# Optimization experiments

Measured on AMD Instinct MI355X. Metric: run time of the kernel, lower is better.

## Reference

```python
import jax, jax.numpy as jnp
import numpy as np

B, N_PER, D_IN, D_OUT, E_PER = 64, 256, 256, 128, 8192  # graphs, nodes/graph, in feat, out feat (=clusters K), edges/graph
EPS = 1e-12


def _sage(h, src, dst, W, b):
    # DenseSAGEConv (mean aggregator): h [n,Din], src/dst [E]
    agg = jnp.zeros_like(h).at[dst].add(h[src])                 # sum of in-neighbor messages
    deg = jnp.zeros((h.shape[0],), h.dtype).at[dst].add(1.0)
    agg = agg / jnp.maximum(deg, 1.0)[:, None]                  # mean aggregation
    z = jnp.concatenate([h, agg], axis=-1) @ W + b              # Linear(2*Din -> Dout)
    z = z / jnp.maximum(jnp.linalg.norm(z, axis=-1, keepdims=True), EPS)  # F.normalize(p=2)
    return jax.nn.relu(z)                                       # activation


def setup_inputs() -> dict:
    key = jax.random.key(0)
    ks = jax.random.split(key, 5)
    h = jax.random.normal(ks[0], (B, N_PER, D_IN), jnp.float32)
    edge_src = jax.random.randint(ks[1], (B, E_PER), 0, N_PER)
    edge_dst = jax.random.randint(ks[2], (B, E_PER), 0, N_PER)
    s = 1.0 / np.sqrt(2 * D_IN)
    W_feat = jax.random.uniform(ks[3], (2 * D_IN, D_OUT), jnp.float32, -s, s)
    b_feat = jnp.zeros((D_OUT,), jnp.float32)
    W_pool = jax.random.uniform(ks[4], (2 * D_IN, D_OUT), jnp.float32, -s, s)
    b_pool = jnp.zeros((D_OUT,), jnp.float32)
    return {"h": h, "edge_src": edge_src, "edge_dst": edge_dst,
            "W_feat": W_feat, "b_feat": b_feat, "W_pool": W_pool, "b_pool": b_pool}


def reference(h, edge_src, edge_dst, W_feat, b_feat, W_pool, b_pool):
    sage = jax.vmap(_sage, in_axes=(0, 0, 0, None, None))
    feat = sage(h, edge_src, edge_dst, W_feat, b_feat)                          # [B,n,K]
    assign = jax.nn.softmax(sage(h, edge_src, edge_dst, W_pool, b_pool), -1)    # [B,n,K]
    # h = assign^T @ feat, per graph (equivalent to block_diag(assign)^T @ stacked feat)
    h_pool = jnp.einsum('bnk,bnd->bkd', assign, feat).reshape(B * D_OUT, D_OUT)  # [B*K, Dout]
    # adj_new = S^T A S per graph; A[dst,src]=1 per edge -> sum_e outer(S[dst_e], S[src_e])
    s_dst = jnp.take_along_axis(assign, edge_dst[:, :, None], axis=1)           # [B,E,K]
    s_src = jnp.take_along_axis(assign, edge_src[:, :, None], axis=1)           # [B,E,K]
    blocks = jnp.einsum('bek,bel->bkl', s_dst, s_src)                           # [B,K,K]
    # cross-graph blocks are exactly zero in the batched graph -> block-diagonal dense adj
    adj_new = jax.scipy.linalg.block_diag(*blocks)                              # [B*K, B*K]
    return adj_new, h_pool
```

## Files before the change

### kernel.cpp

```cpp
#include <hip/hip_runtime.h>
#include <hip/hip_bf16.h>
#include <stdint.h>

#define BG 64
#define NP 256
#define DI 256
#define DO 128
#define EP 8192


typedef __attribute__((ext_vector_type(8))) short short8;
typedef __attribute__((ext_vector_type(4))) short short4v;
typedef __attribute__((ext_vector_type(4))) float float4v;

__device__ __forceinline__ int ldi(const void* p, size_t i, int i64) {
  return i64 ? (int)((const long long*)p)[i] : ((const int*)p)[i];
}

__device__ __forceinline__ short f2b(float x) {
  union { float f; unsigned u; } c; c.f = x;
  unsigned r = c.u + 0x7FFFu + ((c.u >> 16) & 1u);
  return (short)(r >> 16);
}
__device__ __forceinline__ float b2f(short b) {
  union { unsigned u; float f; } c; c.u = ((unsigned)(unsigned short)b) << 16;
  return c.f;
}

__device__ __forceinline__ int vote_i64(const void* esrc) {
  const uint32_t* ew = (const uint32_t*)esrc;
  int i64 = 1;
#pragma unroll
  for (int j = 0; j < 8; ++j)
    if (ew[2 * j + 1] != 0) i64 = 0;
  return i64;
}

__global__ __launch_bounds__(256) void k_scatter(const void* __restrict__ esrc,
                                                 const void* __restrict__ edst,
                                                 float* __restrict__ A,
                                                 short* __restrict__ Abf,
                                                 float* __restrict__ deg) {
  __shared__ float Asl[64][256];
  int b = blockIdx.y, rq = blockIdx.x, t = threadIdx.x;
  float4* Az = (float4*)&Asl[0][0];
  for (int i = t; i < 64 * 256 / 4; i += 256) Az[i] = make_float4(0.f, 0.f, 0.f, 0.f);
  int i64 = vote_i64(esrc);
  __syncthreads();
  const size_t base = (size_t)b * EP;
  for (int e = t; e < EP; e += 256) {
    int si = ldi(esrc, base + e, i64) & (NP - 1);
    int di = ldi(edst, base + e, i64) & (NP - 1);
    if ((di >> 6) == rq) atomicAdd(&Asl[di & 63][si], 1.0f);
  }
  __syncthreads();
  int wv = t >> 6, ln = t & 63;
#pragma unroll
  for (int k = 0; k < 16; ++k) {
    int r = k * 4 + wv;
    float4 v = *(float4*)&Asl[r][ln * 4];
    int gr = rq * 64 + r;
    size_t o = ((size_t)b * NP + gr) * NP + ln * 4;
    *(float4*)&A[o] = v;
    short tmp[4] = { f2b(v.x), f2b(v.y), f2b(v.z), f2b(v.w) };
    *(short4v*)&Abf[o] = *(short4v*)tmp;
    float s = v.x + v.y + v.z + v.w;
    s += __shfl_xor(s, 1);  s += __shfl_xor(s, 2);  s += __shfl_xor(s, 4);
    s += __shfl_xor(s, 8);  s += __shfl_xor(s, 16); s += __shfl_xor(s, 32);
    if (ln == 0) deg[b * NP + gr] = s;
  }
}

__global__ __launch_bounds__(256) void k_htr(const float* __restrict__ h,
                                             short* __restrict__ hThi,
                                             short* __restrict__ hTlo) {
  __shared__ float T[64][65];
  int b = blockIdx.z, n0 = blockIdx.x * 64, f0 = blockIdx.y * 64;
  int t = threadIdx.x;
  int r = t >> 4, c4 = (t & 15) * 4;
#pragma unroll
  for (int i = 0; i < 4; ++i) {
    float4 v = *(const float4*)&h[((size_t)b * NP + n0 + i * 16 + r) * DI + f0 + c4];
    T[i * 16 + r][c4 + 0] = v.x; T[i * 16 + r][c4 + 1] = v.y;
    T[i * 16 + r][c4 + 2] = v.z; T[i * 16 + r][c4 + 3] = v.w;
  }
  __syncthreads();
#pragma unroll
  for (int i = 0; i < 4; ++i) {
    int f = i * 16 + r;
    short hi4[4], lo4[4];
#pragma unroll
    for (int j = 0; j < 4; ++j) {
      float x = T[c4 + j][f];
      short hb = f2b(x);
      hi4[j] = hb;
      lo4[j] = f2b(x - b2f(hb));
    }
    size_t o = ((size_t)b * DI + f0 + f) * NP + n0 + c4;
    *(short4v*)&hThi[o] = *(short4v*)hi4;
    *(short4v*)&hTlo[o] = *(short4v*)lo4;
  }
}

__global__ __launch_bounds__(256) void k_gemm_agg(const short* __restrict__ Abf,
                                                  const short* __restrict__ hThi,
                                                  const short* __restrict__ hTlo,
                                                  const float* __restrict__ deg,
                                                  float* __restrict__ agg) {
  int b = blockIdx.y, r0 = blockIdx.x * 32, t = threadIdx.x;
  int wave = t >> 6, lane = t & 63, rt = wave & 1, fh = wave >> 1;
  int m = lane & 15, q = lane >> 4;
  float4v acc[8];
#pragma unroll
  for (int i = 0; i < 8; ++i) acc[i] = (float4v){0.f, 0.f, 0.f, 0.f};
  const short* Ar = &Abf[((size_t)b * NP + r0 + rt * 16 + m) * NP];
  for (int kc = 0; kc < NP; kc += 32) {
    short8 af = *(const short8*)&Ar[kc + q * 8];
#pragma unroll
    for (int tt = 0; tt < 8; ++tt) {
      int f = fh * 128 + tt * 16 + m;
      short8 bh = *(const short8*)&hThi[((size_t)b * DI + f) * NP + kc + q * 8];
      short8 bl = *(const short8*)&hTlo[((size_t)b * DI + f) * NP + kc + q * 8];
      acc[tt] = __builtin_amdgcn_mfma_f32_16x16x32_bf16(af, bh, acc[tt], 0, 0, 0);
      acc[tt] = __builtin_amdgcn_mfma_f32_16x16x32_bf16(af, bl, acc[tt], 0, 0, 0);
    }
  }
#pragma unroll
  for (int reg = 0; reg < 4; ++reg) {
    int row = r0 + rt * 16 + q * 4 + reg;
    float sc = 1.0f / fmaxf(deg[b * NP + row], 1.0f);
#pragma unroll
    for (int tt = 0; tt < 8; ++tt)
      agg[((size_t)b * NP + row) * DI + fh * 128 + tt * 16 + m] = acc[tt][reg] * sc;
  }
}

__global__ __launch_bounds__(256) void k_wt(const float* __restrict__ Wf,
                                            const float* __restrict__ Wp,
                                            short* __restrict__ Wt) {
  __shared__ __align__(16) float T[32][132];
  int b = blockIdx.x;
  int head = b >> 4;
  int k0 = (b & 15) * 32;
  const float* W = head ? Wp : Wf;
  int t = threadIdx.x;
  {
    int k = t >> 3, fs = (t & 7) * 16;
    const float* src = &W[(size_t)(k0 + k) * DO + fs];
#pragma unroll
    for (int j = 0; j < 4; ++j)
      *(float4*)&T[k][fs + j * 4] = *(const float4*)(src + j * 4);
  }
  __syncthreads();
  int f = t & 127, kh = (t >> 7) * 16;
  __align__(16) short tmp[16];
#pragma unroll
  for (int i = 0; i < 16; ++i) tmp[i] = f2b(T[kh + i][f]);
  short* dst = &Wt[((size_t)head * DO + f) * 512 + k0 + kh];
  *(short8*)dst = *(short8*)&tmp[0];
  *(short8*)(dst + 8) = *(short8*)&tmp[8];
}

__global__ __launch_bounds__(256) void k_zepi_mfma(const float* __restrict__ h,
                                                   const float* __restrict__ agg,
                                                   const short* __restrict__ Wt,
                                                   const float* __restrict__ bfe,
                                                   const float* __restrict__ bpo,
                                                   float* __restrict__ feat,
                                                   float* __restrict__ assign) {
  __shared__ __align__(16) short Xs[32][40];
  int r0 = blockIdx.x * 32;
  int t = threadIdx.x;
  int wave = t >> 6, lane = t & 63;
  int rt = wave & 1, ch = wave >> 1;
  int m = lane & 15, q = lane >> 4;
  float4v acc[8];
#pragma unroll
  for (int i = 0; i < 8; ++i) acc[i] = (float4v){0.f, 0.f, 0.f, 0.f};

  for (int kc = 0; kc < 2 * DI; kc += 32) {
    __syncthreads();
    {
      int r = t >> 3, k4 = (t & 7) * 4;
      const float* src = (kc < DI) ? &h[(size_t)(r0 + r) * DI + kc + k4]
                                   : &agg[(size_t)(r0 + r) * DI + (kc - DI) + k4];
      float4 v = *(const float4*)src;
      Xs[r][k4 + 0] = f2b(v.x); Xs[r][k4 + 1] = f2b(v.y);
      Xs[r][k4 + 2] = f2b(v.z); Xs[r][k4 + 3] = f2b(v.w);
    }
    __syncthreads();
    short8 afrag = *(const short8*)&Xs[rt * 16 + m][q * 8];
#pragma unroll
    for (int tt = 0; tt < 8; ++tt) {
      int n = ch * 128 + tt * 16 + m;
      short8 bfrag = *(const short8*)&Wt[(size_t)n * 512 + kc + q * 8];
      acc[tt] = __builtin_amdgcn_mfma_f32_16x16x32_bf16(afrag, bfrag, acc[tt], 0, 0, 0);
    }
  }

  const float* bp = ch ? bpo : bfe;
  float bias[8];
#pragma unroll
  for (int tt = 0; tt < 8; ++tt) bias[tt] = bp ? bp[tt * 16 + m] : 0.f;
#pragma unroll
  for (int reg = 0; reg < 4; ++reg) {
    int row = r0 + rt * 16 + q * 4 + reg;
    float z[8];
    float ss = 0.f;
#pragma unroll
    for (int tt = 0; tt < 8; ++tt) { z[tt] = acc[tt][reg] + bias[tt]; ss += z[tt] * z[tt]; }
    ss += __shfl_xor(ss, 1); ss += __shfl_xor(ss, 2);
    ss += __shfl_xor(ss, 4); ss += __shfl_xor(ss, 8);
    float inv = 1.0f / fmaxf(sqrtf(ss), 1e-12f);
    float v[8];
#pragma unroll
    for (int tt = 0; tt < 8; ++tt) v[tt] = fmaxf(z[tt] * inv, 0.f);
    if (ch == 0) {
#pragma unroll
      for (int tt = 0; tt < 8; ++tt) feat[(size_t)row * DO + tt * 16 + m] = v[tt];
    } else {
      float mx = v[0];
#pragma unroll
      for (int tt = 1; tt < 8; ++tt) mx = fmaxf(mx, v[tt]);
      mx = fmaxf(mx, __shfl_xor(mx, 1)); mx = fmaxf(mx, __shfl_xor(mx, 2));
      mx = fmaxf(mx, __shfl_xor(mx, 4)); mx = fmaxf(mx, __shfl_xor(mx, 8));
      float e[8], s = 0.f;
#pragma unroll
      for (int tt = 0; tt < 8; ++tt) { e[tt] = __expf(v[tt] - mx); s += e[tt]; }
      s += __shfl_xor(s, 1); s += __shfl_xor(s, 2);
      s += __shfl_xor(s, 4); s += __shfl_xor(s, 8);
      float is = 1.0f / s;
#pragma unroll
      for (int tt = 0; tt < 8; ++tt) assign[(size_t)row * DO + tt * 16 + m] = e[tt] * is;
    }
  }
}

__global__ __launch_bounds__(256) void k_gemm_as(const float* __restrict__ A,
                                                 const float* __restrict__ assign,
                                                 float* __restrict__ AS) {
  __shared__ __align__(16) float As[32][68];
  __shared__ __align__(16) float Bs[32][132];
  int b = blockIdx.y;
  int r0 = blockIdx.x * 64;
  int t = threadIdx.x;
  int tr = t >> 4, tc = t & 15;
  float acc[4][8] = {};
  const float* Ab = A + (size_t)b * NP * NP;
  const float* asb = assign + (size_t)b * NP * DO;
  for (int kc = 0; kc < NP; kc += 32) {
    __syncthreads();
    {
      int r = t >> 2;
      int ks = (t & 3) * 8;
      const float* src = &Ab[(size_t)(r0 + r) * NP + kc + ks];
      float4 v0 = *(const float4*)src;
      float4 v1 = *(const float4*)(src + 4);
      As[ks + 0][r] = v0.x; As[ks + 1][r] = v0.y; As[ks + 2][r] = v0.z; As[ks + 3][r] = v0.w;
      As[ks + 4][r] = v1.x; As[ks + 5][r] = v1.y; As[ks + 6][r] = v1.z; As[ks + 7][r] = v1.w;
    }
    {
      int k = t >> 3;
      int ls = (t & 7) * 16;
      const float* src = &asb[(size_t)(kc + k) * DO + ls];
#pragma unroll
      for (int j = 0; j < 4; ++j)
        *(float4*)&Bs[k][ls + j * 4] = *(const float4*)(src + j * 4);
    }
    __syncthreads();
#pragma unroll
    for (int k = 0; k < 32; ++k) {
      float a[4], ww[8];
      *(float4*)&a[0] = *(const float4*)&As[k][tr * 4];
      *(float4*)&ww[0] = *(const float4*)&Bs[k][tc * 8];
      *(float4*)&ww[4] = *(const float4*)&Bs[k][tc * 8 + 4];
#pragma unroll
      for (int i = 0; i < 4; ++i)
#pragma unroll
        for (int j = 0; j < 8; ++j)
          acc[i][j] += a[i] * ww[j];
    }
  }
#pragma unroll
  for (int i = 0; i < 4; ++i) {
    float* dst = &AS[((size_t)b * NP + r0 + tr * 4 + i) * DO + tc * 8];
    *(float4*)dst = *(float4*)&acc[i][0];
    *(float4*)(dst + 4) = *(float4*)&acc[i][4];
  }
}

__global__ __launch_bounds__(256) void k_pool(const float* __restrict__ assign,
                                              const float* __restrict__ AS,
                                              const float* __restrict__ feat,
                                              float* __restrict__ adj,
                                              float* __restrict__ hpool) {
  __shared__ __align__(16) float Ps[32][68];
  __shared__ __align__(16) float Ys[32][132];
  int b = blockIdx.y;
  int mt = blockIdx.x & 1;
  int which = blockIdx.x >> 1;
  const float* Y = which ? feat : AS;
  int m0 = mt * 64;
  int t = threadIdx.x;
  int tr = t >> 4, tc = t & 15;
  float acc[4][8] = {};
  for (int nc = 0; nc < NP; nc += 32) {
    __syncthreads();
    {
      int n = t >> 3;
      int mseg = (t & 7) * 8;
      const float* src = &assign[((size_t)b * NP + nc + n) * DO + m0 + mseg];
      *(float4*)&Ps[n][mseg] = *(const float4*)src;
      *(float4*)&Ps[n][mseg + 4] = *(const float4*)(src + 4);
    }
    {
      int n = t >> 3;
      int ds = (t & 7) * 16;
      const float* src = &Y[((size_t)b * NP + nc + n) * DO + ds];
#pragma unroll
      for (int j = 0; j < 4; ++j)
        *(float4*)&Ys[n][ds + j * 4] = *(const float4*)(src + j * 4);
    }
    __syncthreads();
#pragma unroll
    for (int n = 0; n < 32; ++n) {
      float a[4], ww[8];
      *(float4*)&a[0] = *(const float4*)&Ps[n][tr * 4];
      *(float4*)&ww[0] = *(const float4*)&Ys[n][tc * 8];
      *(float4*)&ww[4] = *(const float4*)&Ys[n][tc * 8 + 4];
#pragma unroll
      for (int i = 0; i < 4; ++i)
#pragma unroll
        for (int j = 0; j < 8; ++j)
          acc[i][j] += a[i] * ww[j];
    }
  }
  if (which == 0) {
#pragma unroll
    for (int i = 0; i < 4; ++i) {
      float* dst = &adj[(size_t)(b * DO + m0 + tr * 4 + i) * (BG * DO) + b * DO + tc * 8];
      *(float4*)dst = *(float4*)&acc[i][0];
      *(float4*)(dst + 4) = *(float4*)&acc[i][4];
    }
  } else {
#pragma unroll
    for (int i = 0; i < 4; ++i) {
      float* dst = &hpool[((size_t)b * DO + m0 + tr * 4 + i) * DO + tc * 8];
      *(float4*)dst = *(float4*)&acc[i][0];
      *(float4*)(dst + 4) = *(float4*)&acc[i][4];
    }
  }
}

extern "C" void kernel_launch(void* const* d_in, const int* in_sizes, int n_in,
                              void* d_out, int out_size, void* d_ws, size_t ws_size,
                              hipStream_t stream) {
  (void)out_size; (void)ws_size;
  int ih = -1, ie[2] = {-1, -1}, iw[2] = {-1, -1}, ib[2] = {-1, -1};
  int ne = 0, nw = 0, nb = 0;
  for (int i = 0; i < n_in; ++i) {
    long long s = in_sizes[i];
    if (s == (long long)BG * NP * DI) { if (ih < 0) ih = i; }
    else if (s == (long long)BG * EP && ne < 2) ie[ne++] = i;
    else if (s == (long long)2 * DI * DO && nw < 2) iw[nw++] = i;
    else if (s == (long long)DO && nb < 2) ib[nb++] = i;
  }
  if (ih < 0 || ne < 2 || nw < 2) {
    ih = 0;
    ie[0] = (n_in > 1) ? 1 : 0;  ie[1] = (n_in > 2) ? 2 : ie[0];
    iw[0] = (n_in > 3) ? 3 : 0;  iw[1] = (n_in > 5) ? 5 : iw[0];
    ib[0] = (n_in > 4) ? 4 : -1; ib[1] = (n_in > 6) ? 6 : -1;
    nb = (ib[1] >= 0) ? 2 : (ib[0] >= 0 ? 1 : 0);
  }
  const float* h    = (const float*)d_in[ih];
  const void* esrc  = d_in[ie[0]];
  const void* edst  = d_in[ie[1]];
  const float* Wf   = (const float*)d_in[iw[0]];
  const float* Wp   = (const float*)d_in[iw[1]];
  const float* bfe  = (nb >= 1) ? (const float*)d_in[ib[0]] : nullptr;
  const float* bpo  = (nb >= 2) ? (const float*)d_in[ib[1]] : nullptr;

  float* adj   = (float*)d_out;
  float* hpool = (float*)d_out + (size_t)(BG * DO) * (BG * DO);
  const size_t ADJ_BYTES = (size_t)(BG * DO) * (BG * DO) * sizeof(float);

  char* wb = (char*)d_ws;
  float* A      = (float*)wb;
  float* agg    = (float*)(wb + 16777216);
  float* feat   = (float*)(wb + 33554432);
  float* assign = (float*)(wb + 41943040);
  float* AS     = (float*)(wb + 50331648);
  float* deg    = (float*)(wb + 58720256);
  short* Wt     = (short*)(wb + 58720256 + 65536);
  short* Abf    = (short*)(wb + 59047936);
  short* hThi   = (short*)(wb + 67436544);
  short* hTlo   = (short*)(wb + 75825152);

  hipMemsetAsync(adj, 0, ADJ_BYTES, stream);
  k_wt<<<32, 256, 0, stream>>>(Wf, Wp, Wt);
  k_htr<<<dim3(4, 4, BG), 256, 0, stream>>>(h, hThi, hTlo);
  k_scatter<<<dim3(4, BG), 256, 0, stream>>>(esrc, edst, A, Abf, deg);
  k_gemm_agg<<<dim3(8, BG), 256, 0, stream>>>(Abf, hThi, hTlo, deg, agg);
  k_zepi_mfma<<<BG * NP / 32, 256, 0, stream>>>(h, agg, Wt, bfe, bpo, feat, assign);
  k_gemm_as<<<dim3(4, BG), 256, 0, stream>>>(A, assign, AS);
  k_pool<<<dim3(4, BG), 256, 0, stream>>>(assign, AS, feat, adj, hpool);
}
```

Baseline: 464.7 us.

## Move A·S and pooling GEMMs to bf16 split-precision MFMA with transposed layouts

The fp32 FMA-based k_gemm_as and k_pool kernels are replaced with MFMA bf16 kernels. Precision is kept by splitting each operand into hi+lo bf16 pairs, and the zepi epilogue now writes feat and assign as transposed hi/lo bf16 through shared memory. The fp32 adjacency copy is dropped, so the scatter writes only the bf16 matrix, which is exact for small edge counts. This targets the scalar-FMA compute and fp32 memory traffic of the pooling stages. In exchange it adds extra MFMA passes and some precision loss from omitting the lo×lo terms.

```diff
diff --git a/kernel.cpp b/kernel.cpp
--- a/kernel.cpp
+++ b/kernel.cpp
@@ -38,7 +38,6 @@
 
 __global__ __launch_bounds__(256) void k_scatter(const void* __restrict__ esrc,
                                                  const void* __restrict__ edst,
-                                                 float* __restrict__ A,
                                                  short* __restrict__ Abf,
                                                  float* __restrict__ deg) {
   __shared__ float Asl[64][256];
@@ -61,7 +60,6 @@
     float4 v = *(float4*)&Asl[r][ln * 4];
     int gr = rq * 64 + r;
     size_t o = ((size_t)b * NP + gr) * NP + ln * 4;
-    *(float4*)&A[o] = v;
     short tmp[4] = { f2b(v.x), f2b(v.y), f2b(v.z), f2b(v.w) };
     *(short4v*)&Abf[o] = *(short4v*)tmp;
     float s = v.x + v.y + v.z + v.w;
@@ -166,9 +164,12 @@
                                                    const short* __restrict__ Wt,
                                                    const float* __restrict__ bfe,
                                                    const float* __restrict__ bpo,
-                                                   float* __restrict__ feat,
-                                                   float* __restrict__ assign) {
+                                                   short* __restrict__ FtH,
+                                                   short* __restrict__ FtL,
+                                                   short* __restrict__ PtH,
+                                                   short* __restrict__ PtL) {
   __shared__ __align__(16) short Xs[32][40];
+  __shared__ __align__(16) short TT[2][2][128][40];
   int r0 = blockIdx.x * 32;
   int t = threadIdx.x;
   int wave = t >> 6, lane = t & 63;
@@ -204,7 +205,7 @@
   for (int tt = 0; tt < 8; ++tt) bias[tt] = bp ? bp[tt * 16 + m] : 0.f;
 #pragma unroll
   for (int reg = 0; reg < 4; ++reg) {
-    int row = r0 + rt * 16 + q * 4 + reg;
+    int rloc = rt * 16 + q * 4 + reg;
     float z[8];
     float ss = 0.f;
 #pragma unroll
@@ -215,10 +216,7 @@
     float v[8];
 #pragma unroll
     for (int tt = 0; tt < 8; ++tt) v[tt] = fmaxf(z[tt] * inv, 0.f);
-    if (ch == 0) {
-#pragma unroll
-      for (int tt = 0; tt < 8; ++tt) feat[(size_t)row * DO + tt * 16 + m] = v[tt];
-    } else {
+    if (ch == 1) {
       float mx = v[0];
 #pragma unroll
       for (int tt = 1; tt < 8; ++tt) mx = fmaxf(mx, v[tt]);
@@ -231,123 +229,119 @@
       s += __shfl_xor(s, 4); s += __shfl_xor(s, 8);
       float is = 1.0f / s;
 #pragma unroll
-      for (int tt = 0; tt < 8; ++tt) assign[(size_t)row * DO + tt * 16 + m] = e[tt] * is;
-    }
-  }
-}
-
-__global__ __launch_bounds__(256) void k_gemm_as(const float* __restrict__ A,
-                                                 const float* __restrict__ assign,
-                                                 float* __restrict__ AS) {
-  __shared__ __align__(16) float As[32][68];
-  __shared__ __align__(16) float Bs[32][132];
+      for (int tt = 0; tt < 8; ++tt) v[tt] = e[tt] * is;
+    }
+#pragma unroll
+    for (int tt = 0; tt < 8; ++tt) {
+      short hb = f2b(v[tt]);
+      short lb = f2b(v[tt] - b2f(hb));
+      TT[ch][0][tt * 16 + m][rloc] = hb;
+      TT[ch][1][tt * 16 + m][rloc] = lb;
+    }
+  }
+  __syncthreads();
+  int b = r0 >> 8, nl = r0 & 255;
+#pragma unroll
+  for (int it = 0; it < 8; ++it) {
+    int chunk = it * 256 + t;
+    int c = chunk & 3, col = (chunk >> 2) & 127;
+    int hl = (chunk >> 9) & 1, head = chunk >> 10;
+    short* base = head ? (hl ? PtL : PtH) : (hl ? FtL : FtH);
+    short* dst = &base[((size_t)b * DO + col) * NP + nl + c * 8];
+    *(short8*)dst = *(const short8*)&TT[head][hl][col][c * 8];
+  }
+}
+
+__global__ __launch_bounds__(256) void k_gemm_as(const short* __restrict__ Abf,
+                                                 const short* __restrict__ PtH,
+                                                 const short* __restrict__ PtL,
+                                                 short* __restrict__ AStH,
+                                                 short* __restrict__ AStL) {
+  __shared__ __align__(16) short TS[2][128][40];
+  int b = blockIdx.y, n0 = blockIdx.x * 32, t = threadIdx.x;
+  int wave = t >> 6, lane = t & 63, rt = wave & 1, fh = wave >> 1;
+  int m = lane & 15, q = lane >> 4;
+  float4v acc[4];
+#pragma unroll
+  for (int i = 0; i < 4; ++i) acc[i] = (float4v){0.f, 0.f, 0.f, 0.f};
+  const short* Ar = &Abf[((size_t)b * NP + n0 + rt * 16 + m) * NP];
+  for (int kc = 0; kc < NP; kc += 32) {
+    short8 af = *(const short8*)&Ar[kc + q * 8];
+#pragma unroll
+    for (int tt = 0; tt < 4; ++tt) {
+      int j = fh * 64 + tt * 16 + m;
+      short8 bh = *(const short8*)&PtH[((size_t)b * DO + j) * NP + kc + q * 8];
+      short8 bl = *(const short8*)&PtL[((size_t)b * DO + j) * NP + kc + q * 8];
+      acc[tt] = __builtin_amdgcn_mfma_f32_16x16x32_bf16(af, bh, acc[tt], 0, 0, 0);
+      acc[tt] = __builtin_amdgcn_mfma_f32_16x16x32_bf16(af, bl, acc[tt], 0, 0, 0);
+    }
+  }
+#pragma unroll
+  for (int tt = 0; tt < 4; ++tt) {
+#pragma unroll
+    for (int reg = 0; reg < 4; ++reg) {
+      int j = fh * 64 + tt * 16 + m;
+      int nl = rt * 16 + q * 4 + reg;
+      float vv = acc[tt][reg];
+      short hb = f2b(vv);
+      TS[0][j][nl] = hb;
+      TS[1][j][nl] = f2b(vv - b2f(hb));
+    }
+  }
+  __syncthreads();
+#pragma unroll
+  for (int it = 0; it < 4; ++it) {
+    int chunk = it * 256 + t;
+    int c = chunk & 3, col = (chunk >> 2) & 127, hl = chunk >> 9;
+    short* dst = &(hl ? AStL : AStH)[((size_t)b * DO + col) * NP + n0 + c * 8];
+    *(short8*)dst = *(const short8*)&TS[hl][col][c * 8];
+  }
+}
+
+__global__ __launch_bounds__(256) void k_pool2(const short* __restrict__ PtH,
+                                               const short* __restrict__ PtL,
+                                               const short* __restrict__ AStH,
+                                               const short* __restrict__ AStL,
+                                               const short* __restrict__ FtH,
+                                               const short* __restrict__ FtL,
+                                               float* __restrict__ adj,
+                                               float* __restrict__ hpool) {
   int b = blockIdx.y;
-  int r0 = blockIdx.x * 64;
-  int t = threadIdx.x;
-  int tr = t >> 4, tc = t & 15;
-  float acc[4][8] = {};
-  const float* Ab = A + (size_t)b * NP * NP;
-  const float* asb = assign + (size_t)b * NP * DO;
+  int ch2 = blockIdx.x & 1, rh = (blockIdx.x >> 1) & 1, which = blockIdx.x >> 2;
+  const short* YH = which ? FtH : AStH;
+  const short* YL = which ? FtL : AStL;
+  int t = threadIdx.x, wave = t >> 6, lane = t & 63;
+  int m = lane & 15, q = lane >> 4;
+  float4v acc[4];
+#pragma unroll
+  for (int i = 0; i < 4; ++i) acc[i] = (float4v){0.f, 0.f, 0.f, 0.f};
+  int irow = rh * 64 + wave * 16 + m;
+  const short* pah = &PtH[((size_t)b * DO + irow) * NP];
+  const short* pal = &PtL[((size_t)b * DO + irow) * NP];
   for (int kc = 0; kc < NP; kc += 32) {
-    __syncthreads();
-    {
-      int r = t >> 2;
-      int ks = (t & 3) * 8;
-      const float* src = &Ab[(size_t)(r0 + r) * NP + kc + ks];
-      float4 v0 = *(const float4*)src;
-      float4 v1 = *(const float4*)(src + 4);
-      As[ks + 0][r] = v0.x; As[ks + 1][r] = v0.y; As[ks + 2][r] = v0.z; As[ks + 3][r] = v0.w;
-      As[ks + 4][r] = v1.x; As[ks + 5][r] = v1.y; As[ks + 6][r] = v1.z; As[ks + 7][r] = v1.w;
-    }
-    {
-      int k = t >> 3;
-      int ls = (t & 7) * 16;
-      const float* src = &asb[(size_t)(kc + k) * DO + ls];
-#pragma unroll
-      for (int j = 0; j < 4; ++j)
-        *(float4*)&Bs[k][ls + j * 4] = *(const float4*)(src + j * 4);
-    }
-    __syncthreads();
-#pragma unroll
-    for (int k = 0; k < 32; ++k) {
-      float a[4], ww[8];
-      *(float4*)&a[0] = *(const float4*)&As[k][tr * 4];
-      *(float4*)&ww[0] = *(const float4*)&Bs[k][tc * 8];
-      *(float4*)&ww[4] = *(const float4*)&Bs[k][tc * 8 + 4];
-#pragma unroll
-      for (int i = 0; i < 4; ++i)
-#pragma unroll
-        for (int j = 0; j < 8; ++j)
-          acc[i][j] += a[i] * ww[j];
-    }
-  }
-#pragma unroll
-  for (int i = 0; i < 4; ++i) {
-    float* dst = &AS[((size_t)b * NP + r0 + tr * 4 + i) * DO + tc * 8];
-    *(float4*)dst = *(float4*)&acc[i][0];
-    *(float4*)(dst + 4) = *(float4*)&acc[i][4];
-  }
-}
-
-__global__ __launch_bounds__(256) void k_pool(const float* __restrict__ assign,
-                                              const float* __restrict__ AS,
-                                              const float* __restrict__ feat,
-                                              float* __restrict__ adj,
-                                              float* __restrict__ hpool) {
-  __shared__ __align__(16) float Ps[32][68];
-  __shared__ __align__(16) float Ys[32][132];
-  int b = blockIdx.y;
-  int mt = blockIdx.x & 1;
-  int which = blockIdx.x >> 1;
-  const float* Y = which ? feat : AS;
-  int m0 = mt * 64;
-  int t = threadIdx.x;
-  int tr = t >> 4, tc = t & 15;
-  float acc[4][8] = {};
-  for (int nc = 0; nc < NP; nc += 32) {
-    __syncthreads();
-    {
-      int n = t >> 3;
-      int mseg = (t & 7) * 8;
-      const float* src = &assign[((size_t)b * NP + nc + n) * DO + m0 + mseg];
-      *(float4*)&Ps[n][mseg] = *(const float4*)src;
-      *(float4*)&Ps[n][mseg + 4] = *(const float4*)(src + 4);
-    }
-    {
-      int n = t >> 3;
-      int ds = (t & 7) * 16;
-      const float* src = &Y[((size_t)b * NP + nc + n) * DO + ds];
-#pragma unroll
-      for (int j = 0; j < 4; ++j)
-        *(float4*)&Ys[n][ds + j * 4] = *(const float4*)(src + j * 4);
-    }
-    __syncthreads();
-#pragma unroll
-    for (int n = 0; n < 32; ++n) {
-      float a[4], ww[8];
-      *(float4*)&a[0] = *(const float4*)&Ps[n][tr * 4];
-      *(float4*)&ww[0] = *(const float4*)&Ys[n][tc * 8];
-      *(float4*)&ww[4] = *(const float4*)&Ys[n][tc * 8 + 4];
-#pragma unroll
-      for (int i = 0; i < 4; ++i)
-#pragma unroll
-        for (int j = 0; j < 8; ++j)
-          acc[i][j] += a[i] * ww[j];
-    }
-  }
-  if (which == 0) {
-#pragma unroll
-    for (int i = 0; i < 4; ++i) {
-      float* dst = &adj[(size_t)(b * DO + m0 + tr * 4 + i) * (BG * DO) + b * DO + tc * 8];
-      *(float4*)dst = *(float4*)&acc[i][0];
-      *(float4*)(dst + 4) = *(float4*)&acc[i][4];
-    }
-  } else {
-#pragma unroll
-    for (int i = 0; i < 4; ++i) {
-      float* dst = &hpool[((size_t)b * DO + m0 + tr * 4 + i) * DO + tc * 8];
-      *(float4*)dst = *(float4*)&acc[i][0];
-      *(float4*)(dst + 4) = *(float4*)&acc[i][4];
+    short8 ah = *(const short8*)&pah[kc + q * 8];
+    short8 al = *(const short8*)&pal[kc + q * 8];
+#pragma unroll
+    for (int tt = 0; tt < 4; ++tt) {
+      int j = ch2 * 64 + tt * 16 + m;
+      short8 bh = *(const short8*)&YH[((size_t)b * DO + j) * NP + kc + q * 8];
+      short8 bl = *(const short8*)&YL[((size_t)b * DO + j) * NP + kc + q * 8];
+      acc[tt] = __builtin_amdgcn_mfma_f32_16x16x32_bf16(ah, bh, acc[tt], 0, 0, 0);
+      acc[tt] = __builtin_amdgcn_mfma_f32_16x16x32_bf16(al, bh, acc[tt], 0, 0, 0);
+      acc[tt] = __builtin_amdgcn_mfma_f32_16x16x32_bf16(ah, bl, acc[tt], 0, 0, 0);
+    }
+  }
+#pragma unroll
+  for (int tt = 0; tt < 4; ++tt) {
+#pragma unroll
+    for (int reg = 0; reg < 4; ++reg) {
+      int i = rh * 64 + wave * 16 + q * 4 + reg;
+      int j = ch2 * 64 + tt * 16 + m;
+      float vv = acc[tt][reg];
+      if (which == 0)
+        adj[(size_t)(b * DO + i) * (BG * DO) + (size_t)b * DO + j] = vv;
+      else
+        hpool[((size_t)b * DO + i) * DO + j] = vv;
     }
   }
 }
@@ -385,23 +379,25 @@
   const size_t ADJ_BYTES = (size_t)(BG * DO) * (BG * DO) * sizeof(float);
 
   char* wb = (char*)d_ws;
-  float* A      = (float*)wb;
-  float* agg    = (float*)(wb + 16777216);
-  float* feat   = (float*)(wb + 33554432);
-  float* assign = (float*)(wb + 41943040);
-  float* AS     = (float*)(wb + 50331648);
-  float* deg    = (float*)(wb + 58720256);
-  short* Wt     = (short*)(wb + 58720256 + 65536);
-  short* Abf    = (short*)(wb + 59047936);
-  short* hThi   = (short*)(wb + 67436544);
-  short* hTlo   = (short*)(wb + 75825152);
+  float* agg  = (float*)wb;
+  short* Abf  = (short*)(wb + 16777216);
+  short* hThi = (short*)(wb + 25165824);
+  short* hTlo = (short*)(wb + 33554432);
+  short* PtH  = (short*)(wb + 41943040);
+  short* PtL  = (short*)(wb + 46137344);
+  short* FtH  = (short*)(wb + 50331648);
+  short* FtL  = (short*)(wb + 54525952);
+  short* AStH = (short*)(wb + 58720256);
+  short* AStL = (short*)(wb + 62914560);
+  float* deg  = (float*)(wb + 67108864);
+  short* Wt   = (short*)(wb + 67174400);
 
   hipMemsetAsync(adj, 0, ADJ_BYTES, stream);
   k_wt<<<32, 256, 0, stream>>>(Wf, Wp, Wt);
   k_htr<<<dim3(4, 4, BG), 256, 0, stream>>>(h, hThi, hTlo);
-  k_scatter<<<dim3(4, BG), 256, 0, stream>>>(esrc, edst, A, Abf, deg);
+  k_scatter<<<dim3(4, BG), 256, 0, stream>>>(esrc, edst, Abf, deg);
   k_gemm_agg<<<dim3(8, BG), 256, 0, stream>>>(Abf, hThi, hTlo, deg, agg);
-  k_zepi_mfma<<<BG * NP / 32, 256, 0, stream>>>(h, agg, Wt, bfe, bpo, feat, assign);
-  k_gemm_as<<<dim3(4, BG), 256, 0, stream>>>(A, assign, AS);
-  k_pool<<<dim3(4, BG), 256, 0, stream>>>(assign, AS, feat, adj, hpool);
-}
+  k_zepi_mfma<<<BG * NP / 32, 256, 0, stream>>>(h, agg, Wt, bfe, bpo, FtH, FtL, PtH, PtL);
+  k_gemm_as<<<dim3(8, BG), 256, 0, stream>>>(Abf, PtH, PtL, AStH, AStL);
+  k_pool2<<<dim3(8, BG), 256, 0, stream>>>(PtH, PtL, AStH, AStL, FtH, FtL, adj, hpool);
+}
```

Result: faster. 448.1 us (-3.6%).
